# Kernel optimization log

Measured on AMD Instinct MI355X. Metric: run time of the kernel, lower is better.

The kernel has to match this reference:

```python
import jax, jax.numpy as jnp
import numpy as np

B, S, D, L = 32, 4096, 1024, 1

def setup_inputs() -> dict:
    key = jax.random.key(0)
    ks = jax.random.split(key, 9)
    sc = 1.0 / np.sqrt(D)
    return {
        "encoder_outputs": jax.random.normal(ks[0], (B, S, D), jnp.float32),
        "decoder_hidden_state": jax.random.normal(ks[1], (L, B, D), jnp.float32),
        "attn_mask": jax.random.randint(ks[2], (B, S), 0, 2) > 0,
        "Wa_w": jax.random.normal(ks[3], (D, D), jnp.float32) * sc,
        "Wa_b": jax.random.normal(ks[4], (D,), jnp.float32) * sc,
        "Ua_w": jax.random.normal(ks[5], (D, D), jnp.float32) * sc,
        "Ua_b": jax.random.normal(ks[6], (D,), jnp.float32) * sc,
        "Va_w": jax.random.normal(ks[7], (1, D), jnp.float32) * sc,
        "Va_b": jax.random.normal(ks[8], (1,), jnp.float32) * sc,
    }

def reference(encoder_outputs, decoder_hidden_state, attn_mask,
              Wa_w, Wa_b, Ua_w, Ua_b, Va_w, Va_b):
    # Ua(decoder_hidden_state): [L,B,D] -> transpose(0,1) -> [B,L,D] -> keep layer 0 -> [B,1,D]
    dec = jnp.einsum('lbd,ed->lbe', decoder_hidden_state, Ua_w) + Ua_b
    dec = jnp.transpose(dec, (1, 0, 2))[:, 0:1, :]            # [B,1,D]
    # Wa(encoder_outputs): [B,S,D]
    enc = jnp.einsum('bsd,ed->bse', encoder_outputs, Wa_w) + Wa_b
    # scores = Va(tanh(enc + dec)) -> [B,S,1] -> [B,1,S]
    scores = jnp.einsum('bsd,od->bso', jnp.tanh(enc + dec), Va_w) + Va_b
    scores = scores[:, :, 0][:, None, :]                      # [B,1,S]
    scores = jnp.where(attn_mask[:, None, :], scores, -jnp.inf)
    weights = jax.nn.softmax(scores, axis=-1)
    return weights
```

## Files before the change

### kernel.cpp

```cpp
#include <hip/hip_runtime.h>
#include <hip/hip_bf16.h>
#include <math.h>

#define D_DIM 1024
#define S_DIM 4096
#define B_DIM 32
#define M_TOTAL (B_DIM * S_DIM)

#define KQ   128
#define NPH  8

using short8 = __attribute__((ext_vector_type(8))) short;
using f32x4  = __attribute__((ext_vector_type(4))) float;

static __device__ __forceinline__ unsigned short f2bf(float x) {
    unsigned int u = __float_as_uint(x);
    u += 0x7fffu + ((u >> 16) & 1u);
    return (unsigned short)(u >> 16);
}

static __device__ __forceinline__ unsigned int pk2(float lo, float hi) {
    __hip_bfloat162 h = __float22bfloat162_rn(float2{lo, hi});
    unsigned int u; __builtin_memcpy(&u, &h, 4); return u;
}

static __device__ __forceinline__ float fast_tanh(float x) {
    float e2 = __expf(2.0f * x);
    return 1.0f - 2.0f * __builtin_amdgcn_rcpf(e2 + 1.0f);
}

__global__ __launch_bounds__(256) void mask_detect_kernel(
        const unsigned int* __restrict__ m, int* __restrict__ flag) {
    __shared__ unsigned int red[4];
    int t = threadIdx.x;
    unsigned int acc = 0;
    for (int i = t; i < 32768; i += 256) acc |= (m[i] & 0xFFFFFF00u);
    #pragma unroll
    for (int k = 1; k <= 32; k <<= 1) acc |= __shfl_xor(acc, k, 64);
    if ((t & 63) == 0) red[t >> 6] = acc;
    __syncthreads();
    if (t == 0) flag[0] = ((red[0] | red[1] | red[2] | red[3]) != 0) ? 1 : 0;
}

__global__ __launch_bounds__(256) void wconv_kernel(
        const float* __restrict__ W, unsigned short* __restrict__ Wt) {
    int tid  = blockIdx.x * 256 + threadIdx.x;
    int lane = tid & 63;
    int kc   = (tid >> 6) & 31;
    int et   = tid >> 11;
    int e = et * 16 + (lane & 15);
    int k = kc * 32 + (lane >> 4) * 8;
    const float* src = W + (size_t)e * D_DIM + k;
    float4 v0 = *(const float4*)(src);
    float4 v1 = *(const float4*)(src + 4);
    short8 pk;
    pk[0] = (short)f2bf(v0.x); pk[1] = (short)f2bf(v0.y);
    pk[2] = (short)f2bf(v0.z); pk[3] = (short)f2bf(v0.w);
    pk[4] = (short)f2bf(v1.x); pk[5] = (short)f2bf(v1.y);
    pk[6] = (short)f2bf(v1.z); pk[7] = (short)f2bf(v1.w);
    *(short8*)(Wt + (size_t)tid * 8) = pk;
}

__global__ __launch_bounds__(256) void off_kernel(
        const float* __restrict__ h, const float* __restrict__ Uw,
        const float* __restrict__ Ub, const float* __restrict__ Wab,
        float* __restrict__ off) {
    int wg   = blockIdx.x * 4 + (threadIdx.x >> 6);
    int lane = threadIdx.x & 63;
    int b = wg >> 10, e = wg & 1023;
    const float4* h4 = (const float4*)(h + (size_t)b * D_DIM);
    const float4* u4 = (const float4*)(Uw + (size_t)e * D_DIM);
    float s = 0.f;
    #pragma unroll
    for (int c = 0; c < 4; ++c) {
        float4 a = h4[c * 64 + lane];
        float4 w = u4[c * 64 + lane];
        s += a.x * w.x + a.y * w.y + a.z * w.z + a.w * w.w;
    }
    #pragma unroll
    for (int m = 32; m; m >>= 1) s += __shfl_xor(s, m, 64);
    if (lane == 0) off[b * D_DIM + e] = s + Ub[e] + Wab[e];
}

__global__ __launch_bounds__(512, 4) void score_kernel(
        const float* __restrict__ A,
        const unsigned short* __restrict__ Wt,
        const float* __restrict__ off,
        const float* __restrict__ Va,
        float* __restrict__ scores)
{
    __shared__ short As[2][64 * KQ];
    __shared__ float score_lds[64];

    const int bid  = blockIdx.x;
    const int pr   = (bid & 7) * 256 + ((bid >> 3) >> 1);
    const int h    = (bid >> 3) & 1;
    const int row0 = pr * 64;
    const int b    = row0 >> 12;

    const int t = threadIdx.x;
    if (t < 64) score_lds[t] = 0.f;

    const int wave = t >> 6, lane = t & 63;
    const int l15 = lane & 15, lhi = lane >> 4;
    const int e0 = h * 512 + wave * 64;

    const unsigned short* WtB =
        Wt + ((size_t)(h * 32 + wave * 4) * 32) * 512 + (size_t)lane * 8;

    const int sr = t >> 3;
    const int sk = (t & 7) * 16;
    const float* Asrc = A + (size_t)(row0 + sr) * D_DIM + sk;
    const int swz   = (sr & 7) << 3;
    const int sidx0 = sr * KQ + (sk ^ swz);
    const int sidx1 = sr * KQ + ((sk + 8) ^ swz);

    f32x4 acc[4][4];
    #pragma unroll
    for (int rf = 0; rf < 4; ++rf)
        #pragma unroll
        for (int cf = 0; cf < 4; ++cf) acc[rf][cf] = (f32x4){0.f, 0.f, 0.f, 0.f};

    {
        float4 v0 = *(const float4*)(Asrc + 0);
        float4 v1 = *(const float4*)(Asrc + 4);
        float4 v2 = *(const float4*)(Asrc + 8);
        float4 v3 = *(const float4*)(Asrc + 12);
        uint4 o0, o1;
        o0.x = pk2(v0.x, v0.y); o0.y = pk2(v0.z, v0.w);
        o0.z = pk2(v1.x, v1.y); o0.w = pk2(v1.z, v1.w);
        o1.x = pk2(v2.x, v2.y); o1.y = pk2(v2.z, v2.w);
        o1.z = pk2(v3.x, v3.y); o1.w = pk2(v3.z, v3.w);
        *(uint4*)(&As[0][sidx0]) = o0;
        *(uint4*)(&As[0][sidx1]) = o1;
    }
    __syncthreads();

    for (int q = 0; q < NPH; ++q) {
        const int cur = q & 1;

        float4 p0, p1, p2, p3;
        if (q < NPH - 1) {
            const float* nx = Asrc + (q + 1) * KQ;
            p0 = *(const float4*)(nx + 0);
            p1 = *(const float4*)(nx + 4);
            p2 = *(const float4*)(nx + 8);
            p3 = *(const float4*)(nx + 12);
        }

        #pragma unroll
        for (int kk = 0; kk < KQ / 32; ++kk) {
            const int k0 = kk * 32 + lhi * 8;
            const int kglob = q * 4 + kk;
            short8 af[4];
            #pragma unroll
            for (int rf = 0; rf < 4; ++rf) {
                int row = rf * 16 + l15;
                af[rf] = *(const short8*)(&As[cur][row * KQ + (k0 ^ ((row & 7) << 3))]);
            }
            __builtin_amdgcn_s_setprio(1);
            #pragma unroll
            for (int cf = 0; cf < 4; ++cf) {
                short8 bfr = *(const short8*)(WtB + (size_t)(cf * 32 + kglob) * 512);
                #pragma unroll
                for (int rf = 0; rf < 4; ++rf)
                    acc[rf][cf] = __builtin_amdgcn_mfma_f32_16x16x32_bf16(
                        af[rf], bfr, acc[rf][cf], 0, 0, 0);
            }
            __builtin_amdgcn_s_setprio(0);
        }

        if (q < NPH - 1) {
            uint4 o0, o1;
            o0.x = pk2(p0.x, p0.y); o0.y = pk2(p0.z, p0.w);
            o0.z = pk2(p1.x, p1.y); o0.w = pk2(p1.z, p1.w);
            o1.x = pk2(p2.x, p2.y); o1.y = pk2(p2.z, p2.w);
            o1.z = pk2(p3.x, p3.y); o1.w = pk2(p3.z, p3.w);
            *(uint4*)(&As[cur ^ 1][sidx0]) = o0;
            *(uint4*)(&As[cur ^ 1][sidx1]) = o1;
        }
        __syncthreads();
    }

    float sp[4][4];
    #pragma unroll
    for (int rf = 0; rf < 4; ++rf)
        #pragma unroll
        for (int j = 0; j < 4; ++j) sp[rf][j] = 0.f;

    #pragma unroll
    for (int cf = 0; cf < 4; ++cf) {
        int e = e0 + cf * 16 + l15;
        float offv = off[b * D_DIM + e];
        float vav  = Va[e];
        #pragma unroll
        for (int rf = 0; rf < 4; ++rf)
            #pragma unroll
            for (int j = 0; j < 4; ++j) {
                float x = acc[rf][cf][j] + offv;
                sp[rf][j] += fast_tanh(x) * vav;
            }
    }

    #pragma unroll
    for (int rf = 0; rf < 4; ++rf)
        #pragma unroll
        for (int j = 0; j < 4; ++j) {
            float v = sp[rf][j];
            v += __shfl_xor(v, 1, 64);
            v += __shfl_xor(v, 2, 64);
            v += __shfl_xor(v, 4, 64);
            v += __shfl_xor(v, 8, 64);
            if (l15 == 0) atomicAdd(&score_lds[rf * 16 + lhi * 4 + j], v);
        }
    __syncthreads();

    if (t < 64) scores[(size_t)h * M_TOTAL + row0 + t] = score_lds[t];
}

__global__ __launch_bounds__(256) void softmax_kernel(
        const float* __restrict__ scores, const void* __restrict__ mask,
        const int* __restrict__ flag, float* __restrict__ out) {
    __shared__ float red[4];
    const int b = blockIdx.x, t = threadIdx.x;
    const float* s0 = scores + (size_t)b * S_DIM;
    const float* s1 = scores + (size_t)M_TOTAL + (size_t)b * S_DIM;
    const int mode8 = flag[0];

    float v[16];
    float mx = -INFINITY;
    if (mode8) {
        const unsigned char* m = (const unsigned char*)mask + (size_t)b * S_DIM;
        #pragma unroll
        for (int i = 0; i < 16; ++i) {
            int idx = i * 256 + t;
            v[i] = m[idx] ? (s0[idx] + s1[idx]) : -INFINITY;
            mx = fmaxf(mx, v[i]);
        }
    } else {
        const int* m = (const int*)mask + (size_t)b * S_DIM;
        #pragma unroll
        for (int i = 0; i < 16; ++i) {
            int idx = i * 256 + t;
            v[i] = m[idx] ? (s0[idx] + s1[idx]) : -INFINITY;
            mx = fmaxf(mx, v[i]);
        }
    }
    #pragma unroll
    for (int k = 1; k <= 32; k <<= 1) mx = fmaxf(mx, __shfl_xor(mx, k, 64));
    if ((t & 63) == 0) red[t >> 6] = mx;
    __syncthreads();
    mx = fmaxf(fmaxf(red[0], red[1]), fmaxf(red[2], red[3]));
    __syncthreads();

    float sum = 0.f;
    #pragma unroll
    for (int i = 0; i < 16; ++i) {
        v[i] = __expf(v[i] - mx);
        sum += v[i];
    }
    #pragma unroll
    for (int k = 1; k <= 32; k <<= 1) sum += __shfl_xor(sum, k, 64);
    if ((t & 63) == 0) red[t >> 6] = sum;
    __syncthreads();
    sum = red[0] + red[1] + red[2] + red[3];
    float inv = 1.f / sum;
    #pragma unroll
    for (int i = 0; i < 16; ++i) out[(size_t)b * S_DIM + i * 256 + t] = v[i] * inv;
}

extern "C" void kernel_launch(void* const* d_in, const int* in_sizes, int n_in,
                              void* d_out, int out_size, void* d_ws, size_t ws_size,
                              hipStream_t stream) {
    const float* enc  = (const float*)d_in[0];
    const float* dech = (const float*)d_in[1];
    const void*  mask = d_in[2];
    const float* Wa_w = (const float*)d_in[3];
    const float* Wa_b = (const float*)d_in[4];
    const float* Ua_w = (const float*)d_in[5];
    const float* Ua_b = (const float*)d_in[6];
    const float* Va_w = (const float*)d_in[7];
    float* out = (float*)d_out;

    char* ws = (char*)d_ws;
    unsigned short* Wt = (unsigned short*)ws;
    float* off    = (float*)(ws + (1u << 21));
    float* scores = (float*)(ws + (1u << 21) + (1u << 17));
    int*   flag   = (int*)(ws + (1u << 21) + (1u << 17) + (1u << 20));

    hipLaunchKernelGGL(mask_detect_kernel, dim3(1), dim3(256), 0, stream,
                       (const unsigned int*)mask, flag);
    hipLaunchKernelGGL(wconv_kernel, dim3(512), dim3(256), 0, stream, Wa_w, Wt);
    hipLaunchKernelGGL(off_kernel, dim3(8192), dim3(256), 0, stream,
                       dech, Ua_w, Ua_b, Wa_b, off);
    hipLaunchKernelGGL(score_kernel, dim3(4096), dim3(512), 0, stream,
                       enc, Wt, off, Va_w, scores);
    hipLaunchKernelGGL(softmax_kernel, dim3(B_DIM), dim3(256), 0, stream,
                       scores, mask, flag, out);
}
```

Before: 381.7 us.

## Split output columns four ways with register-prefetched B fragments and atomic score reduction

```diff
diff --git a/kernel.cpp b/kernel.cpp
--- a/kernel.cpp
+++ b/kernel.cpp
@@ -82,6 +82,10 @@
     if (lane == 0) off[b * D_DIM + e] = s + Ub[e] + Wab[e];
 }
 
+__global__ __launch_bounds__(256) void zero_kernel(float* __restrict__ p) {
+    ((float4*)p)[blockIdx.x * 256 + threadIdx.x] = (float4){0.f, 0.f, 0.f, 0.f};
+}
+
 __global__ __launch_bounds__(512, 4) void score_kernel(
         const float* __restrict__ A,
         const unsigned short* __restrict__ Wt,
@@ -93,8 +97,8 @@
     __shared__ float score_lds[64];
 
     const int bid  = blockIdx.x;
-    const int pr   = (bid & 7) * 256 + ((bid >> 3) >> 1);
-    const int h    = (bid >> 3) & 1;
+    const int pr   = (bid & 7) * 256 + (bid >> 5);
+    const int qr   = (bid >> 3) & 3;
     const int row0 = pr * 64;
     const int b    = row0 >> 12;
 
@@ -103,10 +107,11 @@
 
     const int wave = t >> 6, lane = t & 63;
     const int l15 = lane & 15, lhi = lane >> 4;
-    const int e0 = h * 512 + wave * 64;
+    const int e0 = qr * 256 + wave * 32;
+    const int c0 = qr * 16 + wave * 2;
 
     const unsigned short* WtB =
-        Wt + ((size_t)(h * 32 + wave * 4) * 32) * 512 + (size_t)lane * 8;
+        Wt + (size_t)c0 * 32 * 512 + (size_t)lane * 8;
 
     const int sr = t >> 3;
     const int sk = (t & 7) * 16;
@@ -115,11 +120,39 @@
     const int sidx0 = sr * KQ + (sk ^ swz);
     const int sidx1 = sr * KQ + ((sk + 8) ^ swz);
 
-    f32x4 acc[4][4];
+    f32x4 acc[4][2];
     #pragma unroll
     for (int rf = 0; rf < 4; ++rf)
         #pragma unroll
-        for (int cf = 0; cf < 4; ++cf) acc[rf][cf] = (f32x4){0.f, 0.f, 0.f, 0.f};
+        for (int cf = 0; cf < 2; ++cf) acc[rf][cf] = (f32x4){0.f, 0.f, 0.f, 0.f};
+
+    short8 B0[2], B1[2], B2[2], B3[2];
+
+    #define LOADB(SET, KG) do {                                              \
+        const int kg_ = (KG) < 31 ? (KG) : 31;                               \
+        SET[0] = *(const short8*)(WtB + (size_t)kg_ * 512);                  \
+        SET[1] = *(const short8*)(WtB + 16384 + (size_t)kg_ * 512);          \
+    } while (0)
+
+    #define MF(KK, USE, PRE) do {                                            \
+        LOADB(PRE, q * 4 + (KK) + 2);                                        \
+        short8 af[4];                                                        \
+        const int k0_ = (KK) * 32 + lhi * 8;                                 \
+        _Pragma("unroll")                                                    \
+        for (int rf = 0; rf < 4; ++rf) {                                     \
+            int row = rf * 16 + l15;                                         \
+            af[rf] = *(const short8*)(&As[cur][row * KQ                      \
+                       + (k0_ ^ ((row & 7) << 3))]);                         \
+        }                                                                    \
+        __builtin_amdgcn_s_setprio(1);                                       \
+        _Pragma("unroll")                                                    \
+        for (int rf = 0; rf < 4; ++rf)                                       \
+            _Pragma("unroll")                                                \
+            for (int cf = 0; cf < 2; ++cf)                                   \
+                acc[rf][cf] = __builtin_amdgcn_mfma_f32_16x16x32_bf16(       \
+                    af[rf], USE[cf], acc[rf][cf], 0, 0, 0);                  \
+        __builtin_amdgcn_s_setprio(0);                                       \
+    } while (0)
 
     {
         float4 v0 = *(const float4*)(Asrc + 0);
@@ -134,12 +167,17 @@
         *(uint4*)(&As[0][sidx0]) = o0;
         *(uint4*)(&As[0][sidx1]) = o1;
     }
+    LOADB(B0, 0);
+    LOADB(B1, 1);
     __syncthreads();
 
     for (int q = 0; q < NPH; ++q) {
         const int cur = q & 1;
-
         float4 p0, p1, p2, p3;
+
+        MF(0, B0, B2);
+        MF(1, B1, B3);
+
         if (q < NPH - 1) {
             const float* nx = Asrc + (q + 1) * KQ;
             p0 = *(const float4*)(nx + 0);
@@ -148,27 +186,8 @@
             p3 = *(const float4*)(nx + 12);
         }
 
-        #pragma unroll
-        for (int kk = 0; kk < KQ / 32; ++kk) {
-            const int k0 = kk * 32 + lhi * 8;
-            const int kglob = q * 4 + kk;
-            short8 af[4];
-            #pragma unroll
-            for (int rf = 0; rf < 4; ++rf) {
-                int row = rf * 16 + l15;
-                af[rf] = *(const short8*)(&As[cur][row * KQ + (k0 ^ ((row & 7) << 3))]);
-            }
-            __builtin_amdgcn_s_setprio(1);
-            #pragma unroll
-            for (int cf = 0; cf < 4; ++cf) {
-                short8 bfr = *(const short8*)(WtB + (size_t)(cf * 32 + kglob) * 512);
-                #pragma unroll
-                for (int rf = 0; rf < 4; ++rf)
-                    acc[rf][cf] = __builtin_amdgcn_mfma_f32_16x16x32_bf16(
-                        af[rf], bfr, acc[rf][cf], 0, 0, 0);
-            }
-            __builtin_amdgcn_s_setprio(0);
-        }
+        MF(2, B2, B0);
+        MF(3, B3, B1);
 
         if (q < NPH - 1) {
             uint4 o0, o1;
@@ -189,7 +208,7 @@
         for (int j = 0; j < 4; ++j) sp[rf][j] = 0.f;
 
     #pragma unroll
-    for (int cf = 0; cf < 4; ++cf) {
+    for (int cf = 0; cf < 2; ++cf) {
         int e = e0 + cf * 16 + l15;
         float offv = off[b * D_DIM + e];
         float vav  = Va[e];
@@ -215,7 +234,7 @@
         }
     __syncthreads();
 
-    if (t < 64) scores[(size_t)h * M_TOTAL + row0 + t] = score_lds[t];
+    if (t < 64) atomicAdd(&scores[row0 + t], score_lds[t]);
 }
 
 __global__ __launch_bounds__(256) void softmax_kernel(
@@ -223,8 +242,7 @@
         const int* __restrict__ flag, float* __restrict__ out) {
     __shared__ float red[4];
     const int b = blockIdx.x, t = threadIdx.x;
-    const float* s0 = scores + (size_t)b * S_DIM;
-    const float* s1 = scores + (size_t)M_TOTAL + (size_t)b * S_DIM;
+    const float* s = scores + (size_t)b * S_DIM;
     const int mode8 = flag[0];
 
     float v[16];
@@ -234,7 +252,7 @@
         #pragma unroll
         for (int i = 0; i < 16; ++i) {
             int idx = i * 256 + t;
-            v[i] = m[idx] ? (s0[idx] + s1[idx]) : -INFINITY;
+            v[i] = m[idx] ? s[idx] : -INFINITY;
             mx = fmaxf(mx, v[i]);
         }
     } else {
@@ -242,7 +260,7 @@
         #pragma unroll
         for (int i = 0; i < 16; ++i) {
             int idx = i * 256 + t;
-            v[i] = m[idx] ? (s0[idx] + s1[idx]) : -INFINITY;
+            v[i] = m[idx] ? s[idx] : -INFINITY;
             mx = fmaxf(mx, v[i]);
         }
     }
@@ -286,14 +304,15 @@
     unsigned short* Wt = (unsigned short*)ws;
     float* off    = (float*)(ws + (1u << 21));
     float* scores = (float*)(ws + (1u << 21) + (1u << 17));
-    int*   flag   = (int*)(ws + (1u << 21) + (1u << 17) + (1u << 20));
+    int*   flag   = (int*)(ws + (1u << 21) + (1u << 17) + (1u << 19));
 
     hipLaunchKernelGGL(mask_detect_kernel, dim3(1), dim3(256), 0, stream,
                        (const unsigned int*)mask, flag);
     hipLaunchKernelGGL(wconv_kernel, dim3(512), dim3(256), 0, stream, Wa_w, Wt);
     hipLaunchKernelGGL(off_kernel, dim3(8192), dim3(256), 0, stream,
                        dech, Ua_w, Ua_b, Wa_b, off);
-    hipLaunchKernelGGL(score_kernel, dim3(4096), dim3(512), 0, stream,
+    hipLaunchKernelGGL(zero_kernel, dim3(128), dim3(256), 0, stream, scores);
+    hipLaunchKernelGGL(score_kernel, dim3(8192), dim3(512), 0, stream,
                        enc, Wt, off, Va_w, scores);
     hipLaunchKernelGGL(softmax_kernel, dim3(B_DIM), dim3(256), 0, stream,
                        scores, mask, flag, out);
```

Measured after the change: 416.7 us. +9.1%, slower.

## Retile score GEMM waves to 2x4 grid with B-fragment register prefetch

Applied to the files above, without the earlier changes.

```diff
diff --git a/kernel.cpp b/kernel.cpp
--- a/kernel.cpp
+++ b/kernel.cpp
@@ -65,24 +65,24 @@
         const float* __restrict__ h, const float* __restrict__ Uw,
         const float* __restrict__ Ub, const float* __restrict__ Wab,
         float* __restrict__ off) {
-    int wg   = blockIdx.x * 4 + (threadIdx.x >> 6);
-    int lane = threadIdx.x & 63;
-    int b = wg >> 10, e = wg & 1023;
-    const float4* h4 = (const float4*)(h + (size_t)b * D_DIM);
-    const float4* u4 = (const float4*)(Uw + (size_t)e * D_DIM);
-    float s = 0.f;
-    #pragma unroll
-    for (int c = 0; c < 4; ++c) {
-        float4 a = h4[c * 64 + lane];
-        float4 w = u4[c * 64 + lane];
-        s += a.x * w.x + a.y * w.y + a.z * w.z + a.w * w.w;
-    }
-    #pragma unroll
-    for (int m = 32; m; m >>= 1) s += __shfl_xor(s, m, 64);
-    if (lane == 0) off[b * D_DIM + e] = s + Ub[e] + Wab[e];
-}
-
-__global__ __launch_bounds__(512, 4) void score_kernel(
+    const int e = blockIdx.x;
+    const int t = threadIdx.x;
+    __shared__ float red[4];
+    float4 u = ((const float4*)(Uw + (size_t)e * D_DIM))[t];
+    float base = Ub[e] + Wab[e];
+    for (int b = 0; b < B_DIM; ++b) {
+        float4 a = ((const float4*)(h + (size_t)b * D_DIM))[t];
+        float s = a.x * u.x + a.y * u.y + a.z * u.z + a.w * u.w;
+        #pragma unroll
+        for (int m = 32; m; m >>= 1) s += __shfl_xor(s, m, 64);
+        if ((t & 63) == 0) red[t >> 6] = s;
+        __syncthreads();
+        if (t == 0) off[b * D_DIM + e] = red[0] + red[1] + red[2] + red[3] + base;
+        __syncthreads();
+    }
+}
+
+__global__ __launch_bounds__(512, 2) void score_kernel(
         const float* __restrict__ A,
         const unsigned short* __restrict__ Wt,
         const float* __restrict__ off,
@@ -94,7 +94,7 @@
 
     const int bid  = blockIdx.x;
     const int pr   = (bid & 7) * 256 + ((bid >> 3) >> 1);
-    const int h    = (bid >> 3) & 1;
+    const int hh   = (bid >> 3) & 1;
     const int row0 = pr * 64;
     const int b    = row0 >> 12;
 
@@ -103,98 +103,117 @@
 
     const int wave = t >> 6, lane = t & 63;
     const int l15 = lane & 15, lhi = lane >> 4;
-    const int e0 = h * 512 + wave * 64;
-
-    const unsigned short* WtB =
-        Wt + ((size_t)(h * 32 + wave * 4) * 32) * 512 + (size_t)lane * 8;
+    const int wr   = wave >> 2;
+    const int wcol = wave & 3;
+    const int e0 = hh * 512 + wcol * 128;
+    const int etb = hh * 32 + wcol * 8;
 
     const int sr = t >> 3;
-    const int sk = (t & 7) * 16;
-    const float* Asrc = A + (size_t)(row0 + sr) * D_DIM + sk;
-    const int swz   = (sr & 7) << 3;
-    const int sidx0 = sr * KQ + (sk ^ swz);
-    const int sidx1 = sr * KQ + ((sk + 8) ^ swz);
-
-    f32x4 acc[4][4];
-    #pragma unroll
-    for (int rf = 0; rf < 4; ++rf)
-        #pragma unroll
-        for (int cf = 0; cf < 4; ++cf) acc[rf][cf] = (f32x4){0.f, 0.f, 0.f, 0.f};
-
-    {
-        float4 v0 = *(const float4*)(Asrc + 0);
-        float4 v1 = *(const float4*)(Asrc + 4);
-        float4 v2 = *(const float4*)(Asrc + 8);
-        float4 v3 = *(const float4*)(Asrc + 12);
-        uint4 o0, o1;
-        o0.x = pk2(v0.x, v0.y); o0.y = pk2(v0.z, v0.w);
-        o0.z = pk2(v1.x, v1.y); o0.w = pk2(v1.z, v1.w);
-        o1.x = pk2(v2.x, v2.y); o1.y = pk2(v2.z, v2.w);
-        o1.z = pk2(v3.x, v3.y); o1.w = pk2(v3.z, v3.w);
-        *(uint4*)(&As[0][sidx0]) = o0;
-        *(uint4*)(&As[0][sidx1]) = o1;
-    }
-    __syncthreads();
-
-    for (int q = 0; q < NPH; ++q) {
-        const int cur = q & 1;
-
-        float4 p0, p1, p2, p3;
-        if (q < NPH - 1) {
-            const float* nx = Asrc + (q + 1) * KQ;
-            p0 = *(const float4*)(nx + 0);
-            p1 = *(const float4*)(nx + 4);
-            p2 = *(const float4*)(nx + 8);
-            p3 = *(const float4*)(nx + 12);
-        }
-
-        #pragma unroll
-        for (int kk = 0; kk < KQ / 32; ++kk) {
-            const int k0 = kk * 32 + lhi * 8;
-            const int kglob = q * 4 + kk;
-            short8 af[4];
-            #pragma unroll
-            for (int rf = 0; rf < 4; ++rf) {
-                int row = rf * 16 + l15;
-                af[rf] = *(const short8*)(&As[cur][row * KQ + (k0 ^ ((row & 7) << 3))]);
-            }
-            __builtin_amdgcn_s_setprio(1);
-            #pragma unroll
-            for (int cf = 0; cf < 4; ++cf) {
-                short8 bfr = *(const short8*)(WtB + (size_t)(cf * 32 + kglob) * 512);
-                #pragma unroll
-                for (int rf = 0; rf < 4; ++rf)
-                    acc[rf][cf] = __builtin_amdgcn_mfma_f32_16x16x32_bf16(
-                        af[rf], bfr, acc[rf][cf], 0, 0, 0);
-            }
-            __builtin_amdgcn_s_setprio(0);
-        }
-
-        if (q < NPH - 1) {
-            uint4 o0, o1;
-            o0.x = pk2(p0.x, p0.y); o0.y = pk2(p0.z, p0.w);
-            o0.z = pk2(p1.x, p1.y); o0.w = pk2(p1.z, p1.w);
-            o1.x = pk2(p2.x, p2.y); o1.y = pk2(p2.z, p2.w);
-            o1.z = pk2(p3.x, p3.y); o1.w = pk2(p3.z, p3.w);
-            *(uint4*)(&As[cur ^ 1][sidx0]) = o0;
-            *(uint4*)(&As[cur ^ 1][sidx1]) = o1;
-        }
-        __syncthreads();
-    }
-
-    float sp[4][4];
-    #pragma unroll
-    for (int rf = 0; rf < 4; ++rf)
+    const int kb = (t & 7) * 16;
+    const float* asrc = A + (size_t)(row0 + sr) * D_DIM + kb;
+    const int sp_ = sr * 2 + (kb >> 6);
+    const int sg0 = ((kb & 63) >> 3);
+    const int sx  = (sp_ & 7) << 4;
+    const int sb0 = sp_ * 128 + ((sg0 * 16) ^ sx);
+    const int sb1 = sp_ * 128 + (((sg0 + 1) * 16) ^ sx);
+
+    f32x4 acc[2][8];
+    #pragma unroll
+    for (int rf = 0; rf < 2; ++rf)
+        #pragma unroll
+        for (int cf = 0; cf < 8; ++cf) acc[rf][cf] = (f32x4){0.f, 0.f, 0.f, 0.f};
+
+    short8 BA[8], BB[8];
+    float4 s0a, s0b, s0c, s0d, s1a, s1b, s1c, s1d;
+
+    #define ISSUE0(Q) do { const float* nx_ = asrc + (Q) * KQ;               \
+        s0a = *(const float4*)(nx_ + 0);  s0b = *(const float4*)(nx_ + 4);   \
+        s0c = *(const float4*)(nx_ + 8);  s0d = *(const float4*)(nx_ + 12); } while (0)
+    #define ISSUE1(Q) do { const float* nx_ = asrc + (Q) * KQ;               \
+        s1a = *(const float4*)(nx_ + 0);  s1b = *(const float4*)(nx_ + 4);   \
+        s1c = *(const float4*)(nx_ + 8);  s1d = *(const float4*)(nx_ + 12); } while (0)
+
+    #define CONVERT(RA, RB, RC, RD, BUF) do {                                \
+        uint4 o0_, o1_;                                                      \
+        o0_.x = pk2(RA.x, RA.y); o0_.y = pk2(RA.z, RA.w);                    \
+        o0_.z = pk2(RB.x, RB.y); o0_.w = pk2(RB.z, RB.w);                    \
+        o1_.x = pk2(RC.x, RC.y); o1_.y = pk2(RC.z, RC.w);                    \
+        o1_.z = pk2(RD.x, RD.y); o1_.w = pk2(RD.z, RD.w);                    \
+        *(uint4*)((char*)As[BUF] + sb0) = o0_;                               \
+        *(uint4*)((char*)As[BUF] + sb1) = o1_; } while (0)
+
+    #define LOADB(SET, KG) do {                                              \
+        const int kg_ = (KG) < 31 ? (KG) : 31;                               \
+        _Pragma("unroll")                                                    \
+        for (int cf = 0; cf < 8; ++cf)                                       \
+            SET[cf] = *(const short8*)(Wt                                    \
+                + ((size_t)((etb + cf) * 32 + kg_)) * 512 + lane * 8);       \
+    } while (0)
+
+    #define KK(Q, K, CUR, LD, USE) do {                                      \
+        LOADB(LD, (Q) * 4 + (K) + 1);                                        \
+        short8 af[2];                                                        \
+        _Pragma("unroll")                                                    \
+        for (int rf = 0; rf < 2; ++rf) {                                     \
+            int r_ = wr * 32 + rf * 16 + l15;                                \
+            int p_ = r_ * 2 + ((K) >> 1);                                    \
+            int g_ = ((K) & 1) * 4 + lhi;                                    \
+            af[rf] = *(const short8*)((const char*)As[CUR]                   \
+                       + p_ * 128 + ((g_ * 16) ^ ((p_ & 7) << 4)));          \
+        }                                                                    \
+        __builtin_amdgcn_s_setprio(1);                                       \
+        _Pragma("unroll")                                                    \
+        for (int rf = 0; rf < 2; ++rf)                                       \
+            _Pragma("unroll")                                                \
+            for (int cf = 0; cf < 8; ++cf)                                   \
+                acc[rf][cf] = __builtin_amdgcn_mfma_f32_16x16x32_bf16(       \
+                    af[rf], USE[cf], acc[rf][cf], 0, 0, 0);                  \
+        __builtin_amdgcn_s_setprio(0);                                       \
+    } while (0)
+
+    #define COMPUTE(Q, CUR) do {                                             \
+        KK(Q, 0, CUR, BB, BA);                                               \
+        KK(Q, 1, CUR, BA, BB);                                               \
+        KK(Q, 2, CUR, BB, BA);                                               \
+        KK(Q, 3, CUR, BA, BB);      \
+    } while (0)
+
+    ISSUE0(0);
+    CONVERT(s0a, s0b, s0c, s0d, 0);
+    ISSUE1(1);
+    LOADB(BA, 0);
+    __syncthreads();
+
+    for (int q2 = 0; q2 < 4; ++q2) {
+        {
+            const int q = 2 * q2;
+            if (q + 2 < NPH) ISSUE0(q + 2);
+            COMPUTE(q, 0);
+            CONVERT(s1a, s1b, s1c, s1d, 1);
+            __syncthreads();
+        }
+        {
+            const int q = 2 * q2 + 1;
+            if (q + 2 < NPH) ISSUE1(q + 2);
+            COMPUTE(q, 1);
+            if (q + 1 < NPH) CONVERT(s0a, s0b, s0c, s0d, 0);
+            __syncthreads();
+        }
+    }
+
+    float sp[2][4];
+    #pragma unroll
+    for (int rf = 0; rf < 2; ++rf)
         #pragma unroll
         for (int j = 0; j < 4; ++j) sp[rf][j] = 0.f;
 
     #pragma unroll
-    for (int cf = 0; cf < 4; ++cf) {
+    for (int cf = 0; cf < 8; ++cf) {
         int e = e0 + cf * 16 + l15;
         float offv = off[b * D_DIM + e];
         float vav  = Va[e];
         #pragma unroll
-        for (int rf = 0; rf < 4; ++rf)
+        for (int rf = 0; rf < 2; ++rf)
             #pragma unroll
             for (int j = 0; j < 4; ++j) {
                 float x = acc[rf][cf][j] + offv;
@@ -203,7 +222,7 @@
     }
 
     #pragma unroll
-    for (int rf = 0; rf < 4; ++rf)
+    for (int rf = 0; rf < 2; ++rf)
         #pragma unroll
         for (int j = 0; j < 4; ++j) {
             float v = sp[rf][j];
@@ -211,11 +230,12 @@
             v += __shfl_xor(v, 2, 64);
             v += __shfl_xor(v, 4, 64);
             v += __shfl_xor(v, 8, 64);
-            if (l15 == 0) atomicAdd(&score_lds[rf * 16 + lhi * 4 + j], v);
-        }
-    __syncthreads();
-
-    if (t < 64) scores[(size_t)h * M_TOTAL + row0 + t] = score_lds[t];
+            if (l15 == 0)
+                atomicAdd(&score_lds[wr * 32 + rf * 16 + lhi * 4 + j], v);
+        }
+    __syncthreads();
+
+    if (t < 64) scores[(size_t)hh * M_TOTAL + row0 + t] = score_lds[t];
 }
 
 __global__ __launch_bounds__(256) void softmax_kernel(
@@ -291,7 +311,7 @@
     hipLaunchKernelGGL(mask_detect_kernel, dim3(1), dim3(256), 0, stream,
                        (const unsigned int*)mask, flag);
     hipLaunchKernelGGL(wconv_kernel, dim3(512), dim3(256), 0, stream, Wa_w, Wt);
-    hipLaunchKernelGGL(off_kernel, dim3(8192), dim3(256), 0, stream,
+    hipLaunchKernelGGL(off_kernel, dim3(1024), dim3(256), 0, stream,
                        dech, Ua_w, Ua_b, Wa_b, off);
     hipLaunchKernelGGL(score_kernel, dim3(4096), dim3(512), 0, stream,
                        enc, Wt, off, Va_w, scores);
```

New measurement: 523.5 us. 1.37x slower.
